# Optimization experiments

Measured on AMD Instinct MI355X. Metric: run time of the kernel, lower is better.

The kernel has to match this reference:

```python
import jax, jax.numpy as jnp
import numpy as np

NUM_HEADS = 8
ATTN_BALANCE = 0.5
EPS = 1e-4  # eps in normalize()


def mp_linear(x, w, gain):
    # MP_Conv with kernel=(1,1): per-output-channel RMS weight renorm then scale.
    # normalize(w): w / (eps + ||w_row|| / sqrt(fan_in)); then * gain / sqrt(fan_in)
    fan_in = w.shape[1]
    n = jnp.linalg.norm(w.astype(jnp.float32), axis=1, keepdims=True)  # (out,1)
    wn = w / (EPS + n / np.sqrt(fan_in))
    wn = wn * (gain / np.sqrt(fan_in))
    return x @ wn.T


def setup_inputs() -> dict:
    key = jax.random.key(0)
    ks = jax.random.split(key, 6)
    B, S, E = 8, 1024, 1024
    H = NUM_HEADS
    return {
        "query": jax.random.normal(ks[0], (B, S, E), jnp.float32),
        "gain_s": jnp.ones((), jnp.float32),
        "gain_t": jnp.ones((), jnp.float32),
        "q_w": jax.random.normal(ks[1], (E, E), jnp.float32),
        "k_w": jax.random.normal(ks[2], (E, E), jnp.float32),
        "v_w": jax.random.normal(ks[3], (E, E), jnp.float32),
        "o_w": jax.random.normal(ks[4], (E, E), jnp.float32),
        "rel_pos_bias": 0.01 * jax.random.normal(ks[5], (H, S, S), jnp.float32),
    }


def reference(query, gain_s, gain_t, q_w, k_w, v_w, o_w, rel_pos_bias):
    # time_dim=0 so the time-dependent branches are inactive; gain_t unused.
    B, S, E = query.shape
    H = NUM_HEADS
    hd = E // H
    # MP projections (1x1 conv == per-position linear), split heads -> (B,H,S,hd)
    q = mp_linear(query, q_w, gain_s).reshape(B, S, H, hd).transpose(0, 2, 1, 3)
    k = mp_linear(query, k_w, gain_s).reshape(B, S, H, hd).transpose(0, 2, 1, 3)
    v = mp_linear(query, v_w, gain_s).reshape(B, S, H, hd).transpose(0, 2, 1, 3)
    # (B,H,S,S) scores, scaled, plus learned relative position bias (seq_len == seq_ln)
    scores = jnp.einsum("bhsd,bhtd->bhst", q, k) / np.sqrt(hd) + rel_pos_bias[None]
    attn = jax.nn.softmax(scores, axis=-1)
    o = jnp.einsum("bhst,bhtd->bhsd", attn, v)
    o = o.transpose(0, 2, 1, 3).reshape(B, S, E)
    out = mp_linear(o, o_w, gain_s)
    # mp_sum residual: lerp(res, out, t) / sqrt((1-t)^2 + t^2)
    t = ATTN_BALANCE
    return (query * (1.0 - t) + out * t) / np.sqrt((1.0 - t) ** 2 + t ** 2)
```

## Files before the change

kernel.cpp:

```cpp
#include <hip/hip_runtime.h>
#include <hip/hip_bf16.h>
#include <math.h>


typedef __attribute__((ext_vector_type(4))) float f32x4;
typedef __attribute__((ext_vector_type(16))) float f32x16;
typedef __attribute__((ext_vector_type(4))) short s16x4;
typedef __attribute__((ext_vector_type(8))) short s16x8;

__device__ __forceinline__ short f2bf(float f) {
  union { __hip_bfloat16 h; short s; } u;
  u.h = __float2bfloat16(f);
  return u.s;
}
__device__ __forceinline__ float bf2f(short s) {
  union { short s; __hip_bfloat16 h; } u;
  u.s = s;
  return __bfloat162float(u.h);
}
__device__ __forceinline__ f32x4 mfma16(s16x8 a, s16x8 b, f32x4 c) {
  return __builtin_amdgcn_mfma_f32_16x16x32_bf16(a, b, c, 0, 0, 0);
}
__device__ __forceinline__ f32x16 mfma32(s16x8 a, s16x8 b, f32x16 c) {
  return __builtin_amdgcn_mfma_f32_32x32x16_bf16(a, b, c, 0, 0, 0);
}

typedef __attribute__((address_space(1))) const unsigned int* as1_u32p;
typedef __attribute__((address_space(3))) unsigned int* as3_u32p;
__device__ __forceinline__ void g2l16(const short* g, short* l) {
  __builtin_amdgcn_global_load_lds((as1_u32p)g, (as3_u32p)l, 16, 0, 0);
}

#define ASM_VMCNT0 asm volatile("s_waitcnt vmcnt(0)" ::: "memory")
#define ASM_VMCNT8 asm volatile("s_waitcnt vmcnt(8)" ::: "memory")
#define ASM_LGKM0  asm volatile("s_waitcnt lgkmcnt(0)" ::: "memory")
#define SFENCE     __builtin_amdgcn_sched_barrier(0)
#define BARRIER    __builtin_amdgcn_s_barrier()

__global__ __launch_bounds__(256) void k_prep(const float* __restrict__ qw, const float* __restrict__ kw,
                                              const float* __restrict__ vw, const float* __restrict__ ow,
                                              const float* __restrict__ gain, const float* __restrict__ query,
                                              const float* __restrict__ bias, short* __restrict__ wn,
                                              short* __restrict__ xq, short* __restrict__ b2) {
  __shared__ float red[256];
  const int bid = blockIdx.x, tid = threadIdx.x;
  if (bid < 4096) {
    const int mat = bid >> 10;
    const float* W = mat == 0 ? qw : mat == 1 ? kw : mat == 2 ? vw : ow;
    const float* src = W + (size_t)(bid & 1023) * 1024;
    f32x4 v = *(const f32x4*)&src[tid * 4];
    float s = v[0]*v[0] + v[1]*v[1] + v[2]*v[2] + v[3]*v[3];
    red[tid] = s; __syncthreads();
    for (int off = 128; off > 0; off >>= 1) {
      if (tid < off) red[tid] += red[tid + off];
      __syncthreads();
    }
    const float scale = gain[0] / (0.0032f + sqrtf(red[0]));
    s16x4 o;
    o[0] = f2bf(v[0]*scale); o[1] = f2bf(v[1]*scale);
    o[2] = f2bf(v[2]*scale); o[3] = f2bf(v[3]*scale);
    *(s16x4*)&wn[(size_t)bid * 1024 + tid * 4] = o;
  } else if (bid < 6144) {
    for (int i = (bid - 4096) * 256 + tid; i < 2097152; i += 524288) {
      f32x4 v = ((const f32x4*)query)[i];
      s16x4 o;
      o[0] = f2bf(v[0]); o[1] = f2bf(v[1]); o[2] = f2bf(v[2]); o[3] = f2bf(v[3]);
      ((s16x4*)xq)[i] = o;
    }
  } else {
    const float L2E = 1.4426950408889634f;
    for (int i = (bid - 6144) * 256 + tid; i < 2097152; i += 524288) {
      f32x4 v = ((const f32x4*)bias)[i];
      s16x4 o;
      o[0] = f2bf(v[0]*L2E); o[1] = f2bf(v[1]*L2E);
      o[2] = f2bf(v[2]*L2E); o[3] = f2bf(v[3]*L2E);
      ((s16x4*)b2)[i] = o;
    }
  }
}

__device__ __forceinline__ void gemm_core(const short* __restrict__ X, const short* __restrict__ W_,
                                          int m0, int n0, int lane, int w, int hi, int ql,
                                          int wm, int wn_, short Al[2][8192], short Bl[2][8192],
                                          f32x4 acc[4][4]) {
  const int srw = lane >> 3, ssl = lane & 7, ql7 = ql & 7;
  auto stage8 = [&](int BI, int K0) {
#pragma unroll
    for (int i = 0; i < 4; i++) {
      const int row = i * 32 + w * 8 + srw;
      g2l16(&X[(size_t)(m0 + row) * 1024 + K0 + ((ssl ^ srw) << 3)],
            &Al[BI][(i * 32 + w * 8) * 64]);
      g2l16(&W_[(size_t)(n0 + row) * 1024 + K0 + ((ssl ^ srw) << 3)],
            &Bl[BI][(i * 32 + w * 8) * 64]);
    }
  };
  auto compute_tile = [&](int BI) {
    const char* alp = (const char*)&Al[BI][0];
    const char* blp = (const char*)&Bl[BI][0];
    __builtin_amdgcn_s_setprio(1);
#pragma unroll
    for (int kc = 0; kc < 2; ++kc) {
      s16x8 af[4], bfr[4];
#pragma unroll
      for (int i = 0; i < 4; i++) {
        const int rA = wm * 64 + i * 16 + ql;
        af[i] = *(const s16x8*)(alp + rA * 128 + ((kc * 64 + 16 * hi) ^ (ql7 << 4)));
      }
#pragma unroll
      for (int j = 0; j < 4; j++) {
        const int rB = wn_ * 64 + j * 16 + ql;
        bfr[j] = *(const s16x8*)(blp + rB * 128 + ((kc * 64 + 16 * hi) ^ (ql7 << 4)));
      }
#pragma unroll
      for (int i = 0; i < 4; i++)
#pragma unroll
        for (int j = 0; j < 4; j++) acc[i][j] = mfma16(af[i], bfr[j], acc[i][j]);
    }
    __builtin_amdgcn_s_setprio(0);
  };
  stage8(0, 0);
  stage8(1, 64);
  int bi = 0;
  for (int t = 0; t < 15; ++t) {
    ASM_VMCNT8; SFENCE; BARRIER; SFENCE;
    compute_tile(bi);
    SFENCE; BARRIER; SFENCE;
    if (t < 14) stage8(bi, (t + 2) * 64);
    bi ^= 1;
  }
  ASM_VMCNT0; SFENCE; BARRIER; SFENCE;
  compute_tile(bi);
}

__global__ __launch_bounds__(256) void k_gemm_qkv(const short* __restrict__ X, const short* __restrict__ WN,
                                                  short* __restrict__ Qb, short* __restrict__ Kb,
                                                  short* __restrict__ Vt) {
  __shared__ short Al[2][128 * 64];
  __shared__ short Bl[2][128 * 64];
  const int z = blockIdx.z;
  const short* __restrict__ Wm = WN + (size_t)z * 1048576;
  const int m0 = blockIdx.x * 128, n0 = blockIdx.y * 128;
  const int tid = threadIdx.x, lane = tid & 63, w = tid >> 6;
  const int hi = lane >> 4, ql = lane & 15;
  const int wm = w >> 1, wn_ = w & 1;
  f32x4 acc[4][4];
#pragma unroll
  for (int i = 0; i < 4; i++)
#pragma unroll
    for (int j = 0; j < 4; j++) acc[i][j] = (f32x4){0.f, 0.f, 0.f, 0.f};
  gemm_core(X, Wm, m0, n0, lane, w, hi, ql, wm, wn_, Al, Bl, acc);
  short* Cl = &Al[0][0];
  if (z == 2) {
#pragma unroll
    for (int i = 0; i < 4; i++) {
#pragma unroll
      for (int j = 0; j < 4; j++) {
        int col = wn_ * 64 + j * 16 + ql;
        int rowb = wm * 64 + i * 16 + 4 * hi;
#pragma unroll
        for (int r = 0; r < 4; r++) Cl[col * 128 + rowb + r] = f2bf(acc[i][j][r]);
      }
    }
    __syncthreads();
    const int b = m0 >> 10, sb = (m0 & 1023);
#pragma unroll
    for (int it = 0; it < 8; ++it) {
      int idx = tid + it * 256;
      int dl = idx >> 4, c = idx & 15;
      int ng = n0 + dl, h = ng >> 7, d = ng & 127;
      *(s16x8*)&Vt[(size_t)((b * 8 + h) * 128 + d) * 1024 + sb + c * 8] =
          *(const s16x8*)&Cl[dl * 128 + c * 8];
    }
  } else {
    short* __restrict__ C = (z == 0) ? Qb : Kb;
#pragma unroll
    for (int i = 0; i < 4; i++) {
#pragma unroll
      for (int j = 0; j < 4; j++) {
        int col = wn_ * 64 + j * 16 + ql;
        int rowb = wm * 64 + i * 16 + 4 * hi;
#pragma unroll
        for (int r = 0; r < 4; r++) Cl[(rowb + r) * 128 + col] = f2bf(acc[i][j][r]);
      }
    }
    __syncthreads();
#pragma unroll
    for (int it = 0; it < 8; ++it) {
      int idx = tid + it * 256;
      int row = idx >> 4, c = idx & 15;
      *(s16x8*)&C[(size_t)(m0 + row) * 1024 + n0 + c * 8] = *(const s16x8*)&Cl[row * 128 + c * 8];
    }
  }
}

__global__ __launch_bounds__(256) void k_attn(const short* __restrict__ Qb, const short* __restrict__ Kb,
                                              const short* __restrict__ Vt, const short* __restrict__ B2,
                                              short* __restrict__ Ob) {
  __shared__ short lds[64 * 128 + 128 * 64];
  short* Kl = lds;
  short* Vl = lds + 64 * 128;
  int f = blockIdx.x + (blockIdx.y << 3);
  f = (f & 7) * 64 + (f >> 3);
  const int bh = f >> 3, b = bh >> 3, h = bh & 7;
  const int q0 = (f & 7) * 128;
  const int tid = threadIdx.x, w = tid >> 6, lane = tid & 63;
  const int l31 = lane & 31, hi2 = lane >> 5, sw = l31 & 7;
  const int qrow = q0 + w * 32 + l31;
  const short* __restrict__ qbase = Qb + (size_t)(b * 1024 + qrow) * 1024 + h * 128;
  s16x8 qf[8];
#pragma unroll
  for (int kc = 0; kc < 8; kc++) qf[kc] = *(const s16x8*)&qbase[kc * 16 + hi2 * 8];
  float lsum = 0.f;
  f32x16 acc[4];
#pragma unroll
  for (int db = 0; db < 4; db++)
#pragma unroll
    for (int r = 0; r < 16; r++) acc[db][r] = 0.f;
  const float sc2 = (float)(0.08838834764831845 * 1.4426950408889634);
  const int krow_ = tid >> 4, kslot = tid & 15;
  const int vrow_ = tid >> 3, vslot = tid & 7;
  const int vks = vslot >> 1, vm = vslot & 1;
  const short* __restrict__ Kg = Kb + (size_t)(b * 1024) * 1024 + h * 128;
  const short* __restrict__ Vg = Vt + (size_t)bh * 128 * 1024;
  const short* __restrict__ Bg = B2 + (size_t)(h * 1024 + qrow) * 1024;

  s16x8 krA[4], vrA[4], krB[4], vrB[4];
#define LOADT(KR, VR, T0)                                                              \
  do {                                                                                 \
    _Pragma("unroll")                                                                  \
    for (int i = 0; i < 4; i++)                                                        \
      KR[i] = *(const s16x8*)&Kg[(size_t)((T0) + i * 16 + krow_) * 1024 + kslot * 8];  \
    _Pragma("unroll")                                                                  \
    for (int i = 0; i < 4; i++)                                                        \
      VR[i] = *(const s16x8*)&Vg[(size_t)(i * 32 + vrow_) * 1024 + (T0) + vslot * 8];  \
  } while (0)

#define STAGE(KR, VR)                                                                  \
  do {                                                                                 \
    _Pragma("unroll")                                                                  \
    for (int i = 0; i < 4; i++) {                                                      \
      int row = i * 16 + krow_;                                                        \
      *(s16x8*)((char*)Kl + row * 256 + ((kslot ^ (row & 7)) << 4)) = KR[i];           \
    }                                                                                  \
    _Pragma("unroll")                                                                  \
    for (int i = 0; i < 4; i++) {                                                      \
      int row = i * 32 + vrow_;                                                        \
      char* vb = (char*)Vl + row * 128;                                                \
      s16x4 lo, hi4;                                                                   \
      lo[0] = VR[i][0]; lo[1] = VR[i][1]; lo[2] = VR[i][2]; lo[3] = VR[i][3];          \
      hi4[0] = VR[i][4]; hi4[1] = VR[i][5]; hi4[2] = VR[i][6]; hi4[3] = VR[i][7];      \
      *(s16x4*)(vb + (((vks * 2) ^ (row & 7)) << 4) + vm * 8) = lo;                    \
      *(s16x4*)(vb + (((vks * 2 + 1) ^ (row & 7)) << 4) + vm * 8) = hi4;               \
    }                                                                                  \
  } while (0)

#define COMPUTE(T0)                                                                    \
  do {                                                                                 \
    s16x4 br[8];                           \
    _Pragma("unroll")                                                                  \
    for (int tb = 0; tb < 2; tb++)                                                     \
      _Pragma("unroll")                                                                \
      for (int u = 0; u < 4; u++)                                                      \
        br[tb * 4 + u] = *(const s16x4*)&Bg[(T0) + tb * 32 + u * 8 + 4 * hi2];         \
    f32x16 st[2];                                                                      \
    __builtin_amdgcn_s_setprio(1);                                                     \
    _Pragma("unroll")                                                                  \
    for (int tb = 0; tb < 2; tb++) {                                                   \
      _Pragma("unroll")                                                                \
      for (int r = 0; r < 16; r++) st[tb][r] = 0.f;                                    \
      _Pragma("unroll")                                                                \
      for (int kc = 0; kc < 8; kc++) {                                                 \
        s16x8 kf = *(const s16x8*)((const char*)Kl + (tb * 32 + l31) * 256 +           \
                                   (((kc * 2 + hi2) ^ sw) << 4));                      \
        st[tb] = mfma32(kf, qf[kc], st[tb]);                                           \
      }                                                                                \
    }                                                                                  \
    __builtin_amdgcn_s_setprio(0);                                                     \
    _Pragma("unroll")                                                                  \
    for (int tb = 0; tb < 2; tb++)                                                     \
      _Pragma("unroll")                                                                \
      for (int r = 0; r < 16; r++) {                                                   \
        float e = exp2f(fmaf(st[tb][r], sc2, bf2f(br[tb * 4 + (r >> 2)][r & 3])));     \
        st[tb][r] = e;                                                                 \
        lsum += e;                                                                     \
      }                                                                                \
    s16x8 pf[4];                  \
    _Pragma("unroll")                                                                  \
    for (int ks = 0; ks < 4; ks++)                                                     \
      _Pragma("unroll")                                                                \
      for (int e = 0; e < 8; e++)                                                      \
        pf[ks][e] = f2bf(st[ks >> 1][(e & 3) + 8 * (ks & 1) + 4 * (e >> 2)]);          \
    __builtin_amdgcn_s_setprio(1);                                                     \
    _Pragma("unroll")                                                                  \
    for (int db = 0; db < 4; db++)                                                     \
      _Pragma("unroll")                                                                \
      for (int ks = 0; ks < 4; ks++) {                                                 \
        s16x8 vf = *(const s16x8*)((const char*)Vl + (db * 32 + l31) * 128 +           \
                                   (((ks * 2 + hi2) ^ sw) << 4));                      \
        acc[db] = mfma32(vf, pf[ks], acc[db]);                                         \
      }                                                                                \
    __builtin_amdgcn_s_setprio(0);                                                     \
  } while (0)

  LOADT(krA, vrA, 0);
  for (int ih = 0; ih < 8; ++ih) {
    const int t0 = ih * 128;
    ASM_VMCNT0; SFENCE;
    STAGE(krA, vrA);
    LOADT(krB, vrB, t0 + 64);
    ASM_LGKM0; SFENCE; BARRIER; SFENCE;
    COMPUTE(t0);
    BARRIER; SFENCE;
    ASM_VMCNT0; SFENCE;
    STAGE(krB, vrB);
    if (ih < 7) LOADT(krA, vrA, t0 + 128);
    ASM_LGKM0; SFENCE; BARRIER; SFENCE;
    COMPUTE(t0 + 64);
    BARRIER; SFENCE;
  }
  lsum += __shfl_xor(lsum, 32);
  const float invl = 1.f / lsum;
  __syncthreads();
  short* Ol = lds;
  const int qloc = w * 32 + l31, qs = qloc & 7;
#pragma unroll
  for (int db = 0; db < 4; db++) {
#pragma unroll
    for (int u = 0; u < 4; u++) {
      int d0 = db * 32 + u * 8 + 4 * hi2;
      s16x4 v;
      v[0] = f2bf(acc[db][4 * u + 0] * invl);
      v[1] = f2bf(acc[db][4 * u + 1] * invl);
      v[2] = f2bf(acc[db][4 * u + 2] * invl);
      v[3] = f2bf(acc[db][4 * u + 3] * invl);
      *(s16x4*)((char*)Ol + qloc * 256 + (((d0 >> 3) ^ qs) << 4) + (d0 & 7) * 2) = v;
    }
  }
  __syncthreads();
#pragma unroll
  for (int it = 0; it < 8; ++it) {
    int idx = tid + it * 256;
    int row = idx >> 4, c = idx & 15;
    s16x8 vv = *(const s16x8*)((const char*)Ol + row * 256 + ((c ^ (row & 7)) << 4));
    *(s16x8*)&Ob[(size_t)(b * 1024 + q0 + row) * 1024 + h * 128 + c * 8] = vv;
  }
#undef LOADT
#undef STAGE
#undef COMPUTE
}

__global__ __launch_bounds__(256) void k_gemm_o(const short* __restrict__ X, const short* __restrict__ Wm,
                                                const float* __restrict__ Qin, float* __restrict__ Out) {
  __shared__ short Al[2][128 * 64];
  __shared__ short Bl[2][128 * 64];
  const int m0 = blockIdx.x * 128, n0 = blockIdx.y * 128;
  const int tid = threadIdx.x, lane = tid & 63, w = tid >> 6;
  const int hi = lane >> 4, ql = lane & 15;
  const int wm = w >> 1, wn_ = w & 1;
  f32x4 acc[4][4];
#pragma unroll
  for (int i = 0; i < 4; i++)
#pragma unroll
    for (int j = 0; j < 4; j++) acc[i][j] = (f32x4){0.f, 0.f, 0.f, 0.f};
  gemm_core(X, Wm, m0, n0, lane, w, hi, ql, wm, wn_, Al, Bl, acc);
#pragma unroll
  for (int i = 0; i < 4; i++) {
    int mg = m0 + wm * 64 + i * 16 + 4 * hi;
#pragma unroll
    for (int j = 0; j < 4; j++) {
      int ng = n0 + wn_ * 64 + j * 16 + ql;
#pragma unroll
      for (int r = 0; r < 4; r++) {
        size_t idx = (size_t)(mg + r) * 1024 + ng;
        Out[idx] = (Qin[idx] + acc[i][j][r]) * 0.7071067811865476f;
      }
    }
  }
}

extern "C" void kernel_launch(void* const* d_in, const int* in_sizes, int n_in,
                              void* d_out, int out_size, void* d_ws, size_t ws_size,
                              hipStream_t stream) {
  (void)in_sizes; (void)n_in; (void)out_size; (void)ws_size;
  const float* query = (const float*)d_in[0];
  const float* gain_s = (const float*)d_in[1];
  const float* qw = (const float*)d_in[3];
  const float* kw = (const float*)d_in[4];
  const float* vw = (const float*)d_in[5];
  const float* ow = (const float*)d_in[6];
  const float* bias = (const float*)d_in[7];
  float* out = (float*)d_out;

  short* ws = (short*)d_ws;
  short* s_wn = ws;
  short* s_x  = s_wn + 4 * 1048576;
  short* s_B2 = s_x + 8388608;
  short* s_Q  = s_B2 + 8388608;
  short* s_K  = s_Q + 8388608;
  short* s_Vt = s_K + 8388608;
  short* s_O  = s_x;

  k_prep<<<dim3(8192), dim3(256), 0, stream>>>(qw, kw, vw, ow, gain_s, query, bias, s_wn, s_x, s_B2);
  k_gemm_qkv<<<dim3(64, 8, 3), dim3(256), 0, stream>>>(s_x, s_wn, s_Q, s_K, s_Vt);
  k_attn<<<dim3(8, 64), dim3(256), 0, stream>>>(s_Q, s_K, s_Vt, s_B2, s_O);
  k_gemm_o<<<dim3(64, 8), dim3(256), 0, stream>>>(s_O, s_wn + 3 * 1048576, query, out);
}
```

Measured before the change: 296.5 us.

## Split attention over key range with merge pass; single-buffer GEMM LDS

Attention is split into two halves along the key dimension (grid z=2). Each half writes an unnormalized bf16 partial output and its row sums, and a new merge kernel adds the halves and normalizes. This doubles the number of attention blocks to raise occupancy and parallelism. In the same change, the GEMM core drops its double-buffered async prefetch pipeline for a single-buffered load/sync/compute loop, which halves LDS use but exposes load latency. Because the softmax uses a fixed max offset, the halves combine by simple sum, at the cost of extra partial-output memory traffic and one more kernel launch.

```diff
diff --git a/kernel.cpp b/kernel.cpp
--- a/kernel.cpp
+++ b/kernel.cpp
@@ -32,7 +32,6 @@
 }
 
 #define ASM_VMCNT0 asm volatile("s_waitcnt vmcnt(0)" ::: "memory")
-#define ASM_VMCNT8 asm volatile("s_waitcnt vmcnt(8)" ::: "memory")
 #define ASM_LGKM0  asm volatile("s_waitcnt lgkmcnt(0)" ::: "memory")
 #define SFENCE     __builtin_amdgcn_sched_barrier(0)
 #define BARRIER    __builtin_amdgcn_s_barrier()
@@ -81,22 +80,20 @@
 
 __device__ __forceinline__ void gemm_core(const short* __restrict__ X, const short* __restrict__ W_,
                                           int m0, int n0, int lane, int w, int hi, int ql,
-                                          int wm, int wn_, short Al[2][8192], short Bl[2][8192],
+                                          int wm, int wn_, short* Al, short* Bl,
                                           f32x4 acc[4][4]) {
   const int srw = lane >> 3, ssl = lane & 7, ql7 = ql & 7;
-  auto stage8 = [&](int BI, int K0) {
+  for (int t = 0; t < 16; ++t) {
+    const int k0 = t * 64;
 #pragma unroll
     for (int i = 0; i < 4; i++) {
       const int row = i * 32 + w * 8 + srw;
-      g2l16(&X[(size_t)(m0 + row) * 1024 + K0 + ((ssl ^ srw) << 3)],
-            &Al[BI][(i * 32 + w * 8) * 64]);
-      g2l16(&W_[(size_t)(n0 + row) * 1024 + K0 + ((ssl ^ srw) << 3)],
-            &Bl[BI][(i * 32 + w * 8) * 64]);
-    }
-  };
-  auto compute_tile = [&](int BI) {
-    const char* alp = (const char*)&Al[BI][0];
-    const char* blp = (const char*)&Bl[BI][0];
+      g2l16(&X[(size_t)(m0 + row) * 1024 + k0 + ((ssl ^ srw) << 3)],
+            &Al[(i * 32 + w * 8) * 64]);
+      g2l16(&W_[(size_t)(n0 + row) * 1024 + k0 + ((ssl ^ srw) << 3)],
+            &Bl[(i * 32 + w * 8) * 64]);
+    }
+    __syncthreads();
     __builtin_amdgcn_s_setprio(1);
 #pragma unroll
     for (int kc = 0; kc < 2; ++kc) {
@@ -104,12 +101,12 @@
 #pragma unroll
       for (int i = 0; i < 4; i++) {
         const int rA = wm * 64 + i * 16 + ql;
-        af[i] = *(const s16x8*)(alp + rA * 128 + ((kc * 64 + 16 * hi) ^ (ql7 << 4)));
+        af[i] = *(const s16x8*)((const char*)Al + rA * 128 + ((kc * 64 + 16 * hi) ^ (ql7 << 4)));
       }
 #pragma unroll
       for (int j = 0; j < 4; j++) {
         const int rB = wn_ * 64 + j * 16 + ql;
-        bfr[j] = *(const s16x8*)(blp + rB * 128 + ((kc * 64 + 16 * hi) ^ (ql7 << 4)));
+        bfr[j] = *(const s16x8*)((const char*)Bl + rB * 128 + ((kc * 64 + 16 * hi) ^ (ql7 << 4)));
       }
 #pragma unroll
       for (int i = 0; i < 4; i++)
@@ -117,26 +114,16 @@
         for (int j = 0; j < 4; j++) acc[i][j] = mfma16(af[i], bfr[j], acc[i][j]);
     }
     __builtin_amdgcn_s_setprio(0);
-  };
-  stage8(0, 0);
-  stage8(1, 64);
-  int bi = 0;
-  for (int t = 0; t < 15; ++t) {
-    ASM_VMCNT8; SFENCE; BARRIER; SFENCE;
-    compute_tile(bi);
-    SFENCE; BARRIER; SFENCE;
-    if (t < 14) stage8(bi, (t + 2) * 64);
-    bi ^= 1;
-  }
-  ASM_VMCNT0; SFENCE; BARRIER; SFENCE;
-  compute_tile(bi);
+    __syncthreads();
+  }
 }
 
 __global__ __launch_bounds__(256) void k_gemm_qkv(const short* __restrict__ X, const short* __restrict__ WN,
                                                   short* __restrict__ Qb, short* __restrict__ Kb,
                                                   short* __restrict__ Vt) {
-  __shared__ short Al[2][128 * 64];
-  __shared__ short Bl[2][128 * 64];
+  __shared__ short lds[16384];
+  short* Al = lds;
+  short* Bl = lds + 8192;
   const int z = blockIdx.z;
   const short* __restrict__ Wm = WN + (size_t)z * 1048576;
   const int m0 = blockIdx.x * 128, n0 = blockIdx.y * 128;
@@ -149,7 +136,7 @@
 #pragma unroll
     for (int j = 0; j < 4; j++) acc[i][j] = (f32x4){0.f, 0.f, 0.f, 0.f};
   gemm_core(X, Wm, m0, n0, lane, w, hi, ql, wm, wn_, Al, Bl, acc);
-  short* Cl = &Al[0][0];
+  short* Cl = lds;
   if (z == 2) {
 #pragma unroll
     for (int i = 0; i < 4; i++) {
@@ -195,10 +182,12 @@
 
 __global__ __launch_bounds__(256) void k_attn(const short* __restrict__ Qb, const short* __restrict__ Kb,
                                               const short* __restrict__ Vt, const short* __restrict__ B2,
-                                              short* __restrict__ Ob) {
+                                              short* __restrict__ Op, float* __restrict__ Ls) {
   __shared__ short lds[64 * 128 + 128 * 64];
   short* Kl = lds;
   short* Vl = lds + 64 * 128;
+  const int split = blockIdx.z;
+  const int tbase = split * 512;
   int f = blockIdx.x + (blockIdx.y << 3);
   f = (f & 7) * 64 + (f >> 3);
   const int bh = f >> 3, b = bh >> 3, h = bh & 7;
@@ -256,7 +245,7 @@
 
 #define COMPUTE(T0)                                                                    \
   do {                                                                                 \
-    s16x4 br[8];                           \
+    s16x4 br[8];                                                                       \
     _Pragma("unroll")                                                                  \
     for (int tb = 0; tb < 2; tb++)                                                     \
       _Pragma("unroll")                                                                \
@@ -284,7 +273,7 @@
         st[tb][r] = e;                                                                 \
         lsum += e;                                                                     \
       }                                                                                \
-    s16x8 pf[4];                  \
+    s16x8 pf[4];                                                                       \
     _Pragma("unroll")                                                                  \
     for (int ks = 0; ks < 4; ks++)                                                     \
       _Pragma("unroll")                                                                \
@@ -302,9 +291,9 @@
     __builtin_amdgcn_s_setprio(0);                                                     \
   } while (0)
 
-  LOADT(krA, vrA, 0);
-  for (int ih = 0; ih < 8; ++ih) {
-    const int t0 = ih * 128;
+  LOADT(krA, vrA, tbase);
+  for (int ih = 0; ih < 4; ++ih) {
+    const int t0 = tbase + ih * 128;
     ASM_VMCNT0; SFENCE;
     STAGE(krA, vrA);
     LOADT(krB, vrB, t0 + 64);
@@ -313,13 +302,13 @@
     BARRIER; SFENCE;
     ASM_VMCNT0; SFENCE;
     STAGE(krB, vrB);
-    if (ih < 7) LOADT(krA, vrA, t0 + 128);
+    if (ih < 3) LOADT(krA, vrA, t0 + 128);
     ASM_LGKM0; SFENCE; BARRIER; SFENCE;
     COMPUTE(t0 + 64);
     BARRIER; SFENCE;
   }
   lsum += __shfl_xor(lsum, 32);
-  const float invl = 1.f / lsum;
+  if (lane < 32) Ls[split * 65536 + bh * 1024 + qrow] = lsum;
   __syncthreads();
   short* Ol = lds;
   const int qloc = w * 32 + l31, qs = qloc & 7;
@@ -329,30 +318,50 @@
     for (int u = 0; u < 4; u++) {
       int d0 = db * 32 + u * 8 + 4 * hi2;
       s16x4 v;
-      v[0] = f2bf(acc[db][4 * u + 0] * invl);
-      v[1] = f2bf(acc[db][4 * u + 1] * invl);
-      v[2] = f2bf(acc[db][4 * u + 2] * invl);
-      v[3] = f2bf(acc[db][4 * u + 3] * invl);
+      v[0] = f2bf(acc[db][4 * u + 0]);
+      v[1] = f2bf(acc[db][4 * u + 1]);
+      v[2] = f2bf(acc[db][4 * u + 2]);
+      v[3] = f2bf(acc[db][4 * u + 3]);
       *(s16x4*)((char*)Ol + qloc * 256 + (((d0 >> 3) ^ qs) << 4) + (d0 & 7) * 2) = v;
     }
   }
   __syncthreads();
+  short* Od = Op + (size_t)split * 8388608;
 #pragma unroll
   for (int it = 0; it < 8; ++it) {
     int idx = tid + it * 256;
     int row = idx >> 4, c = idx & 15;
     s16x8 vv = *(const s16x8*)((const char*)Ol + row * 256 + ((c ^ (row & 7)) << 4));
-    *(s16x8*)&Ob[(size_t)(b * 1024 + q0 + row) * 1024 + h * 128 + c * 8] = vv;
+    *(s16x8*)&Od[(size_t)(b * 1024 + q0 + row) * 1024 + h * 128 + c * 8] = vv;
   }
 #undef LOADT
 #undef STAGE
 #undef COMPUTE
 }
 
+__global__ __launch_bounds__(256) void k_merge(const short* __restrict__ Op, const float* __restrict__ Ls,
+                                               short* __restrict__ O) {
+  for (int g = blockIdx.x * 256 + threadIdx.x; g < 2097152; g += 262144) {
+    const int q_h = g >> 4;
+    const int h = q_h & 7;
+    const int bq = q_h >> 3;
+    const int b = bq >> 10, q = bq & 1023;
+    const int li = (b * 8 + h) * 1024 + q;
+    const float inv = 1.f / (Ls[li] + Ls[65536 + li]);
+    s16x8 p0 = ((const s16x8*)Op)[g];
+    s16x8 p1 = ((const s16x8*)(Op + 8388608))[g];
+    s16x8 o;
+#pragma unroll
+    for (int e = 0; e < 8; e++) o[e] = f2bf((bf2f(p0[e]) + bf2f(p1[e])) * inv);
+    ((s16x8*)O)[g] = o;
+  }
+}
+
 __global__ __launch_bounds__(256) void k_gemm_o(const short* __restrict__ X, const short* __restrict__ Wm,
                                                 const float* __restrict__ Qin, float* __restrict__ Out) {
-  __shared__ short Al[2][128 * 64];
-  __shared__ short Bl[2][128 * 64];
+  __shared__ short lds[16384];
+  short* Al = lds;
+  short* Bl = lds + 8192;
   const int m0 = blockIdx.x * 128, n0 = blockIdx.y * 128;
   const int tid = threadIdx.x, lane = tid & 63, w = tid >> 6;
   const int hi = lane >> 4, ql = lane & 15;
@@ -398,10 +407,13 @@
   short* s_Q  = s_B2 + 8388608;
   short* s_K  = s_Q + 8388608;
   short* s_Vt = s_K + 8388608;
+  short* s_Op = s_Vt + 8388608;
+  float* s_Ls = (float*)(s_Op + 16777216);
   short* s_O  = s_x;
 
   k_prep<<<dim3(8192), dim3(256), 0, stream>>>(qw, kw, vw, ow, gain_s, query, bias, s_wn, s_x, s_B2);
   k_gemm_qkv<<<dim3(64, 8, 3), dim3(256), 0, stream>>>(s_x, s_wn, s_Q, s_K, s_Vt);
-  k_attn<<<dim3(8, 64), dim3(256), 0, stream>>>(s_Q, s_K, s_Vt, s_B2, s_O);
+  k_attn<<<dim3(8, 64, 2), dim3(256), 0, stream>>>(s_Q, s_K, s_Vt, s_B2, s_Op, s_Ls);
+  k_merge<<<dim3(1024), dim3(256), 0, stream>>>(s_Op, s_Ls, s_O);
   k_gemm_o<<<dim3(64, 8), dim3(256), 0, stream>>>(s_O, s_wn + 3 * 1048576, query, out);
 }
```

New measurement: 318.7 us. 7.5% more time.
